# Optimization experiments

Measured on AMD Instinct MI355X. Metric: run time of the kernel, lower is better.

## Reference

```python
import jax, jax.numpy as jnp
import numpy as np
import math

SR = 16000
FFT = 1024
WIN = 640
HOP = 320
NMEL = 40
NCEP = 13
B = 1024
NS = 16000
F_MIN = 0.0
F_MAX = 8000.0
LIFT_L = 22.0
DELTA_N = 2


def _linear_to_mel_weight_matrix(num_mel, num_spec_bins, sr, fmin, fmax):
    # Exact replica of tf.signal.linear_to_mel_weight_matrix (HTK mel scale).
    def hz_to_mel(f):
        return 1127.0 * np.log1p(np.asarray(f, np.float64) / 700.0)
    nyquist = sr / 2.0
    lin_freqs = np.linspace(0.0, nyquist, num_spec_bins)
    spec_mel = hz_to_mel(lin_freqs[1:])[:, None]          # drop DC bin
    edges = np.linspace(hz_to_mel(fmin), hz_to_mel(fmax), num_mel + 2)
    lower, center, upper = edges[:-2], edges[1:-1], edges[2:]
    lower_slope = (spec_mel - lower) / (center - lower)
    upper_slope = (upper - spec_mel) / (upper - center)
    w = np.maximum(0.0, np.minimum(lower_slope, upper_slope))
    w = np.pad(w, ((1, 0), (0, 0)))                       # re-add zero DC row
    return w.astype(np.float32)


def setup_inputs() -> dict:
    key = jax.random.key(0)
    waveforms = jax.random.normal(key, (B, NS), dtype=jnp.float32)
    mel_fb = jnp.asarray(_linear_to_mel_weight_matrix(NMEL, FFT // 2 + 1, SR, F_MIN, F_MAX))
    return {"waveforms": waveforms, "mel_fb": mel_fb}


def _delta(feat, N):
    # feat: (B, T, C). Replicate-pad N frames at both ends, then weighted
    # sliding-window sum with weights k in [-N..N] (vectorized, no map_fn).
    T = feat.shape[1]
    denom = 2.0 * sum(float(k * k) for k in range(1, N + 1))
    padded = jnp.concatenate(
        [jnp.repeat(feat[:, :1, :], N, axis=1), feat,
         jnp.repeat(feat[:, -1:, :], N, axis=1)], axis=1)
    acc = jnp.zeros_like(feat)
    for k in range(-N, N + 1):
        if k != 0:
            acc = acc + float(k) * padded[:, N + k:N + k + T, :]
    return acc / denom


def reference(waveforms, mel_fb):
    # --- STFT (tf.signal.stft: periodic Hann, no pad_end, zero-pad to FFT) ---
    n = jnp.arange(WIN, dtype=jnp.float32)
    window = 0.5 - 0.5 * jnp.cos(2.0 * math.pi * n / WIN)
    num_frames = 1 + (NS - WIN) // HOP                    # 49
    idx = jnp.arange(num_frames)[:, None] * HOP + jnp.arange(WIN)[None, :]
    frames = waveforms[:, idx] * window
    frames = jnp.pad(frames, ((0, 0), (0, 0), (0, FFT - WIN)))
    spec = jnp.abs(jnp.fft.rfft(frames, n=FFT, axis=-1))  # (B, T, 513)

    # --- mel + log ---
    log_mel = jnp.log(spec @ mel_fb + 1e-6)               # (B, T, NMEL)

    # --- MFCC: DCT-II scaled by rsqrt(2*NMEL), keep first NCEP coeffs ---
    m = jnp.arange(NMEL, dtype=jnp.float32)[:, None]
    k = jnp.arange(NCEP, dtype=jnp.float32)[None, :]
    dct_mat = 2.0 * jnp.cos(math.pi * (2.0 * m + 1.0) * k / (2.0 * NMEL))
    mfccs = (log_mel @ dct_mat) * (1.0 / math.sqrt(2.0 * NMEL))

    # --- liftering ---
    c = jnp.arange(NCEP, dtype=jnp.float32)
    lift = 1.0 + (LIFT_L / 2.0) * jnp.sin(math.pi * c / LIFT_L)
    mfccs = mfccs * lift

    # --- deltas and delta-deltas ---
    d1 = _delta(mfccs, DELTA_N)
    d2 = _delta(d1, DELTA_N)
    out = jnp.concatenate([mfccs, d1, d2], axis=2)        # (B, T, 3*NCEP)
    return out[..., None]                                 # (B, T, 39, 1)
```

## Files before the change

kernel.cpp:

```cpp
#include <hip/hip_runtime.h>
#include <math.h>

#define NMEL   40
#define NCEP   13
#define BATCH  1024
#define NSAMP  16000
#define NFRAME 49
#define PI_F   3.14159265358979323846f

#define WS_WIN  0
#define WS_R    640
#define WS_DT   1664
#define WS_BT   2184
#define WS_TOT  15240
#define SENT0   0x4D464343u
#define SENT1   0x9A7C55E1u

typedef _Float16 half8 __attribute__((ext_vector_type(8)));
typedef __fp16   fp16x2 __attribute__((ext_vector_type(2)));
typedef float f32x4 __attribute__((ext_vector_type(4)));
typedef float f32x2 __attribute__((ext_vector_type(2)));

#define FFT_SB() __builtin_amdgcn_sched_barrier(0x77)

__device__ __forceinline__ f32x2 cmulw(f32x2 d, float wr, float wi) {
    f32x2 sw; sw.x = -d.y; sw.y = d.x;
    return d * wr + sw * wi;
}
#define BFLYC(i0, i1, wr, wi) {            \
    f32x2 dif = zc[i0] - zc[i1];           \
    zc[i0] = zc[i0] + zc[i1];              \
    zc[i1] = cmulw(dif, (wr), (wi)); }

__device__ __forceinline__ unsigned pk_f16(float a, float b) {
    fp16x2 h = __builtin_amdgcn_cvt_pkrtz(a, b);
    union { fp16x2 h; unsigned u; } cvt; cvt.h = h;
    return cvt.u;
}

__global__ __launch_bounds__(256) void mfcc_prep(
    const float* __restrict__ mel_fb, float* __restrict__ ws, int use_sent)
{
    if (use_sent) {
        const unsigned* sw = (const unsigned*)ws;
        if (sw[WS_TOT] == SENT0 && sw[WS_TOT + 1] == SENT1) return;
    }

    const int idx = blockIdx.x * 256 + threadIdx.x;

    _Float16* bt = (_Float16*)(ws + WS_BT);
    for (int i = idx; i < 48 * 544; i += 64 * 256) {
        int n = i / 544, k = i - n * 544;
        float v = (n < NMEL && k < 513) ? mel_fb[k * NMEL + n] : 0.0f;
        bt[i] = (_Float16)v;
    }

    if (idx < 640 + 512 + 520) {
        int i = idx;
        if (i < 640) {
            ws[WS_WIN + i] = 0.5f - 0.5f * cosf(2.0f * PI_F * (float)i / 640.0f);
        } else if (i < 1152) {
            int k = i - 640;
            float s, c;
            sincosf(-2.0f * PI_F * (float)k / 1024.0f, &s, &c);
            ((float2*)(ws + WS_R))[k] = make_float2(c, s);
        } else {
            int j = i - 1152;
            int m = j / 13, c0 = j - m * 13;
            float d    = 2.0f * cosf(PI_F * (2.0f * m + 1.0f) * (float)c0 / 80.0f);
            float lift = 1.0f + 11.0f * sinf(PI_F * (float)c0 / 22.0f);
            ws[WS_DT + j] = d * 0.11180339887498949f * lift;
        }
    }

    if (use_sent && idx == 0) {
        unsigned* sw = (unsigned*)ws;
        sw[WS_TOT]     = SENT0;
        sw[WS_TOT + 1] = SENT1;
    }
}

__device__ __forceinline__ void ldFrame(float2 (&x)[5], const float* __restrict__ wave,
                                        int frame, int L)
{
    const int b = frame / NFRAME;
    const int f = frame - b * NFRAME;
    const float2* xp = (const float2*)(wave + (size_t)b * NSAMP + (size_t)f * 320);
    #pragma unroll
    for (int j = 0; j < 5; ++j) x[j] = xp[L + 64 * j];
}

__device__ __forceinline__ void phaseI(f32x2 (&zc)[8],
    const float2 (&xv)[5], const float2 (&winv)[5],
    const float2 (&twA)[4], const float2 (&twB)[2], const float2 twC)
{
    #pragma unroll
    for (int j = 0; j < 8; ++j) { zc[j].x = 0.0f; zc[j].y = 0.0f; }
    #pragma unroll
    for (int j = 0; j < 5; ++j) {
        f32x2 x; x.x = xv[j].x;   x.y = xv[j].y;
        f32x2 w; w.x = winv[j].x; w.y = winv[j].y;
        zc[j] = x * w;
    }
    #pragma unroll
    for (int j = 0; j < 4; ++j) BFLYC(j, j + 4, twA[j].x, twA[j].y);
    #pragma unroll
    for (int g = 0; g < 8; g += 4) {
        #pragma unroll
        for (int j = 0; j < 2; ++j) BFLYC(g + j, g + j + 2, twB[j].x, twB[j].y);
    }
    #pragma unroll
    for (int i0 = 0; i0 < 8; i0 += 2) BFLYC(i0, i0 + 1, twC.x, twC.y);
}

__device__ __forceinline__ void phaseII(f32x2 (&zc)[8],
    const float4 (&q)[4],
    const float2 (&twD)[4], const float2 (&twE)[2], const float2 twF)
{
    zc[0].x = q[0].x; zc[0].y = q[0].y; zc[1].x = q[0].z; zc[1].y = q[0].w;
    zc[2].x = q[1].x; zc[2].y = q[1].y; zc[3].x = q[1].z; zc[3].y = q[1].w;
    zc[4].x = q[2].x; zc[4].y = q[2].y; zc[5].x = q[2].z; zc[5].y = q[2].w;
    zc[6].x = q[3].x; zc[6].y = q[3].y; zc[7].x = q[3].z; zc[7].y = q[3].w;
    #pragma unroll
    for (int j = 0; j < 4; ++j) BFLYC(j, j + 4, twD[j].x, twD[j].y);
    #pragma unroll
    for (int g = 0; g < 8; g += 4) {
        #pragma unroll
        for (int j = 0; j < 2; ++j) BFLYC(g + j, g + j + 2, twE[j].x, twE[j].y);
    }
    #pragma unroll
    for (int i0 = 0; i0 < 8; i0 += 2) BFLYC(i0, i0 + 1, twF.x, twF.y);
}

__device__ __forceinline__ void phaseIII(f32x2 (&zc)[8], const float4 (&q)[4])
{
    zc[0].x = q[0].x; zc[0].y = q[0].y; zc[1].x = q[0].z; zc[1].y = q[0].w;
    zc[2].x = q[1].x; zc[2].y = q[1].y; zc[3].x = q[1].z; zc[3].y = q[1].w;
    zc[4].x = q[2].x; zc[4].y = q[2].y; zc[5].x = q[2].z; zc[5].y = q[2].w;
    zc[6].x = q[3].x; zc[6].y = q[3].y; zc[7].x = q[3].z; zc[7].y = q[3].w;
    const float C = 0.70710678118654752f;
    const float w8r[4] = { 1.0f,  C, 0.0f, -C };
    const float w8i[4] = { 0.0f, -C, -1.0f, -C };
    #pragma unroll
    for (int j = 0; j < 4; ++j) BFLYC(j, j + 4, w8r[j], w8i[j]);
    #pragma unroll
    for (int g = 0; g < 8; g += 4) {
        BFLYC(g + 0, g + 2, 1.0f, 0.0f);
        BFLYC(g + 1, g + 3, 0.0f, -1.0f);
    }
    #pragma unroll
    for (int i0 = 0; i0 < 8; i0 += 2) BFLYC(i0, i0 + 1, 1.0f, 0.0f);
}

__device__ __forceinline__ void wrEx1(float2* Z, const f32x2 (&zc)[8], int s, int a)
{
    #pragma unroll
    for (int j = 0; j < 8; ++j) Z[80 * j + 10 * s + a] = make_float2(zc[j].x, zc[j].y);
}

__device__ __forceinline__ void wrEx2(float2* Z, const f32x2 (&zc)[8], int s, int a)
{
    #pragma unroll
    for (int j = 0; j < 8; ++j) Z[80 * a + 10 * j + s] = make_float2(zc[j].x, zc[j].y);
}

__device__ __forceinline__ void wrEx3(float2* Z, const f32x2 (&zc)[8], int u)
{
    const int rev3t[8] = { 0, 4, 2, 6, 1, 5, 3, 7 };
    #pragma unroll
    for (int j = 0; j < 8; ++j) Z[80 * rev3t[j] + u] = make_float2(zc[j].x, zc[j].y);
}

__device__ __forceinline__ void rdEx(const float2* Z, int L, float4 (&q)[4])
{
    q[0] = *(const float4*)&Z[10 * L + 0];
    q[1] = *(const float4*)&Z[10 * L + 2];
    q[2] = *(const float4*)&Z[10 * L + 4];
    q[3] = *(const float4*)&Z[10 * L + 6];
}

__device__ __forceinline__ void rdMag(const float2* Z, int L,
    float4 (&aq)[4], float4 (&tq)[4], float2& b0)
{
    aq[0] = *(const float4*)&Z[10 * L + 0];
    aq[1] = *(const float4*)&Z[10 * L + 2];
    aq[2] = *(const float4*)&Z[10 * L + 4];
    aq[3] = *(const float4*)&Z[10 * L + 6];
    tq[0] = *(const float4*)&Z[630 - 10 * L + 0];
    tq[1] = *(const float4*)&Z[630 - 10 * L + 2];
    tq[2] = *(const float4*)&Z[630 - 10 * L + 4];
    tq[3] = *(const float4*)&Z[630 - 10 * L + 6];
    b0    = Z[640 - 10 * L];
}

__device__ __forceinline__ void magPhase(const float4 (&aq)[4], const float4 (&tq)[4],
    const float2 b0, const float2 (&twS)[8], const int L, uint4& mgpo, float& m512o)
{
    float Ax[8], Ay[8], Bx[8], By[8];
    Ax[0] = aq[0].x; Ay[0] = aq[0].y; Ax[1] = aq[0].z; Ay[1] = aq[0].w;
    Ax[2] = aq[1].x; Ay[2] = aq[1].y; Ax[3] = aq[1].z; Ay[3] = aq[1].w;
    Ax[4] = aq[2].x; Ay[4] = aq[2].y; Ax[5] = aq[2].z; Ay[5] = aq[2].w;
    Ax[6] = aq[3].x; Ay[6] = aq[3].y; Ax[7] = aq[3].z; Ay[7] = aq[3].w;
    Bx[0] = b0.x;    By[0] = b0.y;
    Bx[7] = tq[0].z; By[7] = tq[0].w;
    Bx[6] = tq[1].x; By[6] = tq[1].y;
    Bx[5] = tq[1].z; By[5] = tq[1].w;
    Bx[4] = tq[2].x; By[4] = tq[2].y;
    Bx[3] = tq[2].z; By[3] = tq[2].w;
    Bx[2] = tq[3].x; By[2] = tq[3].y;
    Bx[1] = tq[3].z; By[1] = tq[3].w;
    float mg[8];
    #pragma unroll
    for (int j = 0; j < 8; ++j) {
        float xer = 0.5f * (Ax[j] + Bx[j]), xei = 0.5f * (Ay[j] - By[j]);
        float xo  = 0.5f * (Ay[j] + By[j]), xoi = -0.5f * (Ax[j] - Bx[j]);
        float xr = xer + twS[j].x * xo - twS[j].y * xoi;
        float xi = xei + twS[j].x * xoi + twS[j].y * xo;
        mg[j] = __builtin_amdgcn_sqrtf(xr * xr + xi * xi);
    }
    if (L == 0) {
        mg[0]  = fabsf(Ax[0] + Ay[0]);
        m512o  = fabsf(Ax[0] - Ay[0]);
    }
    mgpo.x = pk_f16(mg[0], mg[1]);
    mgpo.y = pk_f16(mg[2], mg[3]);
    mgpo.z = pk_f16(mg[4], mg[5]);
    mgpo.w = pk_f16(mg[6], mg[7]);
}

__global__ __launch_bounds__(256) void mfcc_stage1(
    const float* __restrict__ wave, const float* __restrict__ ws,
    float* __restrict__ out)
{
    __shared__ __align__(16) char smem[4 * 640 * 8 + 16];
    char* smemc = smem;
    _Float16* lm = (_Float16*)(smem + 16 * 1104);

    const int tid = threadIdx.x;
    const int wv  = tid >> 6;
    const int L   = tid & 63;
    const int s   = L & 7;
    const int a   = L >> 3;

    float2* Z = (float2*)smem + wv * 640;
    const float2* R   = (const float2*)(ws + WS_R);
    const float2* win = (const float2*)(ws + WS_WIN);

    float2 twA[4], twB[2], twC, twD[4], twE[2], twF, twS[8], winv[5];
    #pragma unroll
    for (int j = 0; j < 4; ++j) twA[j] = R[2 * (L + 64 * j)];
    #pragma unroll
    for (int j = 0; j < 2; ++j) twB[j] = R[4 * (L + 64 * j)];
    twC = R[8 * L];
    #pragma unroll
    for (int j = 0; j < 4; ++j) twD[j] = R[128 * j + 16 * s];
    #pragma unroll
    for (int j = 0; j < 2; ++j) twE[j] = R[256 * j + 32 * s];
    twF = R[64 * s];
    #pragma unroll
    for (int j = 0; j < 8; ++j) twS[j] = R[8 * L + j];
    #pragma unroll
    for (int j = 0; j < 5; ++j) winv[j] = win[L + 64 * j];

    const int r6 = (int)(__brev((unsigned)L) >> 26);
    const int u  = r6 + 2 * (r6 >> 3);

    uint4 mgp0, mgp1, mgp2, mgp3;
    float m5120 = 0.0f, m5121 = 0.0f, m5122 = 0.0f, m5123 = 0.0f;

    const int fbase = blockIdx.x * 16 + wv * 4;

    float2 xA[5], xB[5];
    ldFrame(xA, wave, fbase + 0, L);
    ldFrame(xB, wave, fbase + 1, L);

    #pragma unroll 1
    for (int p = 0; p < 2; ++p) {
        float2 xA2[5], xB2[5];
        if (p == 0) {
            ldFrame(xA2, wave, fbase + 2, L);
            ldFrame(xB2, wave, fbase + 3, L);
        }

        f32x2 zcA[8], zcB[8];
        float4 qA[4], qB[4];

        phaseI(zcA, xA, winv, twA, twB, twC);
        FFT_SB();
        wrEx1(Z, zcA, s, a);
        FFT_SB();
        rdEx(Z, L, qA);
        FFT_SB();
        phaseI(zcB, xB, winv, twA, twB, twC);
        wrEx1(Z, zcB, s, a);
        FFT_SB();
        rdEx(Z, L, qB);
        FFT_SB();

        phaseII(zcA, qA, twD, twE, twF);
        wrEx2(Z, zcA, s, a);
        FFT_SB();
        rdEx(Z, L, qA);
        FFT_SB();
        phaseII(zcB, qB, twD, twE, twF);
        wrEx2(Z, zcB, s, a);
        FFT_SB();
        rdEx(Z, L, qB);
        FFT_SB();

        phaseIII(zcA, qA);
        wrEx3(Z, zcA, u);
        FFT_SB();
        float4 aqA[4], tqA[4]; float2 b0A;
        rdMag(Z, L, aqA, tqA, b0A);
        FFT_SB();
        phaseIII(zcB, qB);
        wrEx3(Z, zcB, u);
        FFT_SB();
        float4 aqB[4], tqB[4]; float2 b0B;
        rdMag(Z, L, aqB, tqB, b0B);
        FFT_SB();

        uint4 mgA, mgB;
        float mA = 0.0f, mB = 0.0f;
        magPhase(aqA, tqA, b0A, twS, L, mgA, mA);
        magPhase(aqB, tqB, b0B, twS, L, mgB, mB);
        FFT_SB();

        mgp0 = mgp2;  mgp1 = mgp3;  mgp2 = mgA;  mgp3 = mgB;
        m5120 = m5122; m5121 = m5123; m5122 = mA; m5123 = mB;

        if (p == 0) {
            #pragma unroll
            for (int j = 0; j < 5; ++j) { xA[j] = xA2[j]; xB[j] = xB2[j]; }
        }
    }

    __syncthreads();
    {
        const int row = wv * 4;
        *(uint4*)(smemc + (row + 0) * 1104 + 16 * L) = mgp0;
        *(uint4*)(smemc + (row + 1) * 1104 + 16 * L) = mgp1;
        *(uint4*)(smemc + (row + 2) * 1104 + 16 * L) = mgp2;
        *(uint4*)(smemc + (row + 3) * 1104 + 16 * L) = mgp3;
        if (L < 20) {
            unsigned v0 = (L == 0) ? pk_f16(m5120, 0.0f) : 0u;
            unsigned v1 = (L == 0) ? pk_f16(m5121, 0.0f) : 0u;
            unsigned v2 = (L == 0) ? pk_f16(m5122, 0.0f) : 0u;
            unsigned v3 = (L == 0) ? pk_f16(m5123, 0.0f) : 0u;
            *(unsigned*)(smemc + (row + 0) * 1104 + 1024 + 4 * L) = v0;
            *(unsigned*)(smemc + (row + 1) * 1104 + 1024 + 4 * L) = v1;
            *(unsigned*)(smemc + (row + 2) * 1104 + 1024 + 4 * L) = v2;
            *(unsigned*)(smemc + (row + 3) * 1104 + 1024 + 4 * L) = v3;
        }
    }
    __syncthreads();

    if (wv < 3) {
        const int nl = L & 15, q = L >> 4;
        const char* ap = smemc + nl * 1104 + q * 16;
        const _Float16* btp = (const _Float16*)(ws + WS_BT)
                              + (size_t)(wv * 16 + nl) * 544 + q * 8;
        f32x4 acc = {0.0f, 0.0f, 0.0f, 0.0f};
        #pragma unroll
        for (int kk = 0; kk < 17; ++kk) {
            half8 av = *(const half8*)(ap + kk * 64);
            half8 bv = *(const half8*)(btp + kk * 32);
            acc = __builtin_amdgcn_mfma_f32_16x16x32_f16(av, bv, acc, 0, 0, 0);
        }
        const int mel = wv * 16 + nl;
        if (mel < NMEL) {
            #pragma unroll
            for (int r = 0; r < 4; ++r) {
                int fl = q * 4 + r;
                lm[fl * NMEL + mel] = (_Float16)__logf(acc[r] + 1e-6f);
            }
        }
    }
    __syncthreads();

    if (tid < 16 * NCEP) {
        const int fl = tid / NCEP, c = tid - fl * NCEP;
        float acc = 0.0f;
        #pragma unroll
        for (int m = 0; m < NMEL; ++m)
            acc += (float)lm[fl * NMEL + m] * ws[WS_DT + m * 13 + c];
        out[(size_t)(blockIdx.x * 16 + fl) * (3 * NCEP) + c] = acc;
    }
}

__global__ __launch_bounds__(256) void mfcc_stage2(float* __restrict__ out)
{
    #define TC (NFRAME * NCEP)
    __shared__ float xs [4][TC];
    __shared__ float d1s[4][TC];

    const int wv = threadIdx.x >> 6;
    const int L  = threadIdx.x & 63;
    const int b  = blockIdx.x * 4 + wv;

    float* xw  = xs[wv];
    float* d1w = d1s[wv];
    const size_t obase = (size_t)b * NFRAME * (3 * NCEP);

    for (int i = L; i < TC; i += 64) {
        const int t = i / NCEP, c = i - t * NCEP;
        xw[i] = out[obase + t * (3 * NCEP) + c];
    }
    FFT_SB();

    for (int i = L; i < TC; i += 64) {
        const int t = i / NCEP, c = i - t * NCEP;
        float acc = 0.0f;
        #pragma unroll
        for (int k = -2; k <= 2; ++k) {
            if (k == 0) continue;
            int tt = t + k;
            tt = tt < 0 ? 0 : (tt > NFRAME - 1 ? NFRAME - 1 : tt);
            acc += (float)k * xw[tt * NCEP + c];
        }
        float d1 = acc * 0.1f;
        d1w[i] = d1;
        out[obase + t * (3 * NCEP) + NCEP + c] = d1;
    }
    FFT_SB();

    for (int i = L; i < TC; i += 64) {
        const int t = i / NCEP, c = i - t * NCEP;
        float acc = 0.0f;
        #pragma unroll
        for (int k = -2; k <= 2; ++k) {
            if (k == 0) continue;
            int tt = t + k;
            tt = tt < 0 ? 0 : (tt > NFRAME - 1 ? NFRAME - 1 : tt);
            acc += (float)k * d1w[tt * NCEP + c];
        }
        out[obase + t * (3 * NCEP) + 2 * NCEP + c] = acc * 0.1f;
    }
    #undef TC
}

extern "C" void kernel_launch(void* const* d_in, const int* in_sizes, int n_in,
                              void* d_out, int out_size, void* d_ws, size_t ws_size,
                              hipStream_t stream)
{
    const float* wave   = (const float*)d_in[0];
    const float* mel_fb = (const float*)d_in[1];
    float* out = (float*)d_out;
    float* ws  = (float*)d_ws;

    const int use_sent = (ws_size >= (size_t)(WS_TOT + 2) * 4) ? 1 : 0;

    mfcc_prep<<<64, 256, 0, stream>>>(mel_fb, ws, use_sent);
    mfcc_stage1<<<(BATCH * NFRAME) / 16, 256, 0, stream>>>(wave, ws, out);
    mfcc_stage2<<<BATCH / 4, 256, 0, stream>>>(out);
}
```

Baseline: 157.0 us.

## Compute FFT twiddles and window on the fly and process one frame at a time

Stops loading twiddle factors and the Hann window from the workspace into registers and computes them inline with hardware sin/cos intrinsics. The loop now handles one frame per iteration instead of two interleaved frames, and each frame's magnitudes go straight to a separate shared-memory region rather than being held in registers until the end. Launch bounds ask for 4 blocks per CU. The aim is to cut register pressure and raise occupancy, at the cost of more transcendental instructions, more shared memory, less instruction-level parallelism and slightly lower twiddle accuracy.

```diff
diff --git a/kernel.cpp b/kernel.cpp
--- a/kernel.cpp
+++ b/kernel.cpp
@@ -16,6 +16,14 @@
 #define SENT0   0x4D464343u
 #define SENT1   0x9A7C55E1u
 
+#define INV16    0.0625f
+#define INV32    0.03125f
+#define INV64    0.015625f
+#define INV128   0.0078125f
+#define INV256   0.00390625f
+#define INV512   0.001953125f
+#define INV1024  0.0009765625f
+
 typedef _Float16 half8 __attribute__((ext_vector_type(8)));
 typedef __fp16   fp16x2 __attribute__((ext_vector_type(2)));
 typedef float f32x4 __attribute__((ext_vector_type(4)));
@@ -36,6 +44,10 @@
     fp16x2 h = __builtin_amdgcn_cvt_pkrtz(a, b);
     union { fp16x2 h; unsigned u; } cvt; cvt.h = h;
     return cvt.u;
+}
+
+__device__ __forceinline__ float2 twid(float rev) {
+    return make_float2(__builtin_amdgcn_cosf(rev), __builtin_amdgcn_sinf(rev));
 }
 
 __global__ __launch_bounds__(256) void mfcc_prep(
@@ -90,46 +102,62 @@
     for (int j = 0; j < 5; ++j) x[j] = xp[L + 64 * j];
 }
 
-__device__ __forceinline__ void phaseI(f32x2 (&zc)[8],
-    const float2 (&xv)[5], const float2 (&winv)[5],
-    const float2 (&twA)[4], const float2 (&twB)[2], const float2 twC)
-{
+__device__ __forceinline__ void phaseIc(f32x2 (&zc)[8], const float2 (&xv)[5], int L)
+{
+    const float nb = (float)L;
     #pragma unroll
     for (int j = 0; j < 8; ++j) { zc[j].x = 0.0f; zc[j].y = 0.0f; }
     #pragma unroll
     for (int j = 0; j < 5; ++j) {
-        f32x2 x; x.x = xv[j].x;   x.y = xv[j].y;
-        f32x2 w; w.x = winv[j].x; w.y = winv[j].y;
-        zc[j] = x * w;
-    }
-    #pragma unroll
-    for (int j = 0; j < 4; ++j) BFLYC(j, j + 4, twA[j].x, twA[j].y);
-    #pragma unroll
-    for (int g = 0; g < 8; g += 4) {
-        #pragma unroll
-        for (int j = 0; j < 2; ++j) BFLYC(g + j, g + j + 2, twB[j].x, twB[j].y);
-    }
-    #pragma unroll
-    for (int i0 = 0; i0 < 8; i0 += 2) BFLYC(i0, i0 + 1, twC.x, twC.y);
-}
-
-__device__ __forceinline__ void phaseII(f32x2 (&zc)[8],
-    const float4 (&q)[4],
-    const float2 (&twD)[4], const float2 (&twE)[2], const float2 twF)
+        float n2 = (float)(L + 64 * j) * (1.0f / 320.0f);
+        float wx = 0.5f - 0.5f * __builtin_amdgcn_cosf(n2);
+        float wy = 0.5f - 0.5f * __builtin_amdgcn_cosf(n2 + (1.0f / 640.0f));
+        zc[j].x = xv[j].x * wx;
+        zc[j].y = xv[j].y * wy;
+    }
+    const float a0 = -nb * INV512;
+    #pragma unroll
+    for (int j = 0; j < 4; ++j) {
+        float2 w = twid(a0 - 0.125f * (float)j);
+        BFLYC(j, j + 4, w.x, w.y);
+    }
+    const float b0r = -nb * INV256;
+    {
+        float2 w0 = twid(b0r), w1 = twid(b0r - 0.25f);
+        BFLYC(0, 2, w0.x, w0.y); BFLYC(1, 3, w1.x, w1.y);
+        BFLYC(4, 6, w0.x, w0.y); BFLYC(5, 7, w1.x, w1.y);
+    }
+    {
+        float2 wc = twid(-nb * INV128);
+        #pragma unroll
+        for (int i0 = 0; i0 < 8; i0 += 2) BFLYC(i0, i0 + 1, wc.x, wc.y);
+    }
+}
+
+__device__ __forceinline__ void phaseIIc(f32x2 (&zc)[8], const float4 (&q)[4], int s)
 {
     zc[0].x = q[0].x; zc[0].y = q[0].y; zc[1].x = q[0].z; zc[1].y = q[0].w;
     zc[2].x = q[1].x; zc[2].y = q[1].y; zc[3].x = q[1].z; zc[3].y = q[1].w;
     zc[4].x = q[2].x; zc[4].y = q[2].y; zc[5].x = q[2].z; zc[5].y = q[2].w;
     zc[6].x = q[3].x; zc[6].y = q[3].y; zc[7].x = q[3].z; zc[7].y = q[3].w;
-    #pragma unroll
-    for (int j = 0; j < 4; ++j) BFLYC(j, j + 4, twD[j].x, twD[j].y);
-    #pragma unroll
-    for (int g = 0; g < 8; g += 4) {
-        #pragma unroll
-        for (int j = 0; j < 2; ++j) BFLYC(g + j, g + j + 2, twE[j].x, twE[j].y);
-    }
-    #pragma unroll
-    for (int i0 = 0; i0 < 8; i0 += 2) BFLYC(i0, i0 + 1, twF.x, twF.y);
+    const float fs = (float)s;
+    const float d0 = -fs * INV64;
+    #pragma unroll
+    for (int j = 0; j < 4; ++j) {
+        float2 w = twid(d0 - 0.125f * (float)j);
+        BFLYC(j, j + 4, w.x, w.y);
+    }
+    const float e0 = -fs * INV32;
+    {
+        float2 w0 = twid(e0), w1 = twid(e0 - 0.25f);
+        BFLYC(0, 2, w0.x, w0.y); BFLYC(1, 3, w1.x, w1.y);
+        BFLYC(4, 6, w0.x, w0.y); BFLYC(5, 7, w1.x, w1.y);
+    }
+    {
+        float2 wf = twid(-fs * INV16);
+        #pragma unroll
+        for (int i0 = 0; i0 < 8; i0 += 2) BFLYC(i0, i0 + 1, wf.x, wf.y);
+    }
 }
 
 __device__ __forceinline__ void phaseIII(f32x2 (&zc)[8], const float4 (&q)[4])
@@ -194,7 +222,7 @@
 }
 
 __device__ __forceinline__ void magPhase(const float4 (&aq)[4], const float4 (&tq)[4],
-    const float2 b0, const float2 (&twS)[8], const int L, uint4& mgpo, float& m512o)
+    const float2 b0, const int L, uint4& mgpo, float& m512o)
 {
     float Ax[8], Ay[8], Bx[8], By[8];
     Ax[0] = aq[0].x; Ay[0] = aq[0].y; Ax[1] = aq[0].z; Ay[1] = aq[0].w;
@@ -209,13 +237,15 @@
     Bx[3] = tq[2].z; By[3] = tq[2].w;
     Bx[2] = tq[3].x; By[2] = tq[3].y;
     Bx[1] = tq[3].z; By[1] = tq[3].w;
+    const float s0 = -(float)L * INV128;
     float mg[8];
     #pragma unroll
     for (int j = 0; j < 8; ++j) {
+        float2 tws = twid(s0 - (float)j * INV1024);
         float xer = 0.5f * (Ax[j] + Bx[j]), xei = 0.5f * (Ay[j] - By[j]);
         float xo  = 0.5f * (Ay[j] + By[j]), xoi = -0.5f * (Ax[j] - Bx[j]);
-        float xr = xer + twS[j].x * xo - twS[j].y * xoi;
-        float xi = xei + twS[j].x * xoi + twS[j].y * xo;
+        float xr = xer + tws.x * xo - tws.y * xoi;
+        float xi = xei + tws.x * xoi + tws.y * xo;
         mg[j] = __builtin_amdgcn_sqrtf(xr * xr + xi * xi);
     }
     if (L == 0) {
@@ -228,13 +258,13 @@
     mgpo.w = pk_f16(mg[6], mg[7]);
 }
 
-__global__ __launch_bounds__(256) void mfcc_stage1(
+__global__ __launch_bounds__(256, 4) void mfcc_stage1(
     const float* __restrict__ wave, const float* __restrict__ ws,
     float* __restrict__ out)
 {
-    __shared__ __align__(16) char smem[4 * 640 * 8 + 16];
-    char* smemc = smem;
-    _Float16* lm = (_Float16*)(smem + 16 * 1104);
+    __shared__ __align__(16) char smem[20480 + 16 + 16 * 1104 + 16 * 40 * 2];
+    char* magc = smem + 20496;
+    _Float16* lm = (_Float16*)(smem + 20496 + 17664);
 
     const int tid = threadIdx.x;
     const int wv  = tid >> 6;
@@ -243,124 +273,55 @@
     const int a   = L >> 3;
 
     float2* Z = (float2*)smem + wv * 640;
-    const float2* R   = (const float2*)(ws + WS_R);
-    const float2* win = (const float2*)(ws + WS_WIN);
-
-    float2 twA[4], twB[2], twC, twD[4], twE[2], twF, twS[8], winv[5];
-    #pragma unroll
-    for (int j = 0; j < 4; ++j) twA[j] = R[2 * (L + 64 * j)];
-    #pragma unroll
-    for (int j = 0; j < 2; ++j) twB[j] = R[4 * (L + 64 * j)];
-    twC = R[8 * L];
-    #pragma unroll
-    for (int j = 0; j < 4; ++j) twD[j] = R[128 * j + 16 * s];
-    #pragma unroll
-    for (int j = 0; j < 2; ++j) twE[j] = R[256 * j + 32 * s];
-    twF = R[64 * s];
-    #pragma unroll
-    for (int j = 0; j < 8; ++j) twS[j] = R[8 * L + j];
-    #pragma unroll
-    for (int j = 0; j < 5; ++j) winv[j] = win[L + 64 * j];
 
     const int r6 = (int)(__brev((unsigned)L) >> 26);
     const int u  = r6 + 2 * (r6 >> 3);
 
-    uint4 mgp0, mgp1, mgp2, mgp3;
-    float m5120 = 0.0f, m5121 = 0.0f, m5122 = 0.0f, m5123 = 0.0f;
-
     const int fbase = blockIdx.x * 16 + wv * 4;
 
-    float2 xA[5], xB[5];
-    ldFrame(xA, wave, fbase + 0, L);
-    ldFrame(xB, wave, fbase + 1, L);
+    float2 xv[5];
+    ldFrame(xv, wave, fbase, L);
 
     #pragma unroll 1
-    for (int p = 0; p < 2; ++p) {
-        float2 xA2[5], xB2[5];
-        if (p == 0) {
-            ldFrame(xA2, wave, fbase + 2, L);
-            ldFrame(xB2, wave, fbase + 3, L);
-        }
-
-        f32x2 zcA[8], zcB[8];
-        float4 qA[4], qB[4];
-
-        phaseI(zcA, xA, winv, twA, twB, twC);
-        FFT_SB();
-        wrEx1(Z, zcA, s, a);
-        FFT_SB();
-        rdEx(Z, L, qA);
-        FFT_SB();
-        phaseI(zcB, xB, winv, twA, twB, twC);
-        wrEx1(Z, zcB, s, a);
-        FFT_SB();
-        rdEx(Z, L, qB);
-        FFT_SB();
-
-        phaseII(zcA, qA, twD, twE, twF);
-        wrEx2(Z, zcA, s, a);
-        FFT_SB();
-        rdEx(Z, L, qA);
-        FFT_SB();
-        phaseII(zcB, qB, twD, twE, twF);
-        wrEx2(Z, zcB, s, a);
-        FFT_SB();
-        rdEx(Z, L, qB);
-        FFT_SB();
-
-        phaseIII(zcA, qA);
-        wrEx3(Z, zcA, u);
-        FFT_SB();
-        float4 aqA[4], tqA[4]; float2 b0A;
-        rdMag(Z, L, aqA, tqA, b0A);
-        FFT_SB();
-        phaseIII(zcB, qB);
-        wrEx3(Z, zcB, u);
-        FFT_SB();
-        float4 aqB[4], tqB[4]; float2 b0B;
-        rdMag(Z, L, aqB, tqB, b0B);
-        FFT_SB();
-
-        uint4 mgA, mgB;
-        float mA = 0.0f, mB = 0.0f;
-        magPhase(aqA, tqA, b0A, twS, L, mgA, mA);
-        magPhase(aqB, tqB, b0B, twS, L, mgB, mB);
-        FFT_SB();
-
-        mgp0 = mgp2;  mgp1 = mgp3;  mgp2 = mgA;  mgp3 = mgB;
-        m5120 = m5122; m5121 = m5123; m5122 = mA; m5123 = mB;
-
-        if (p == 0) {
-            #pragma unroll
-            for (int j = 0; j < 5; ++j) { xA[j] = xA2[j]; xB[j] = xB2[j]; }
-        }
+    for (int fi = 0; fi < 4; ++fi) {
+        f32x2 zc[8];
+        phaseIc(zc, xv, L);
+        FFT_SB();
+        wrEx1(Z, zc, s, a);
+        FFT_SB();
+        if (fi < 3) ldFrame(xv, wave, fbase + fi + 1, L);
+        float4 q[4];
+        rdEx(Z, L, q);
+        FFT_SB();
+        phaseIIc(zc, q, s);
+        wrEx2(Z, zc, s, a);
+        FFT_SB();
+        rdEx(Z, L, q);
+        FFT_SB();
+        phaseIII(zc, q);
+        wrEx3(Z, zc, u);
+        FFT_SB();
+        float4 aq[4], tq[4]; float2 b0;
+        rdMag(Z, L, aq, tq, b0);
+        FFT_SB();
+        uint4 mg; float m512 = 0.0f;
+        magPhase(aq, tq, b0, L, mg, m512);
+        char* mrow = magc + (wv * 4 + fi) * 1104;
+        *(uint4*)(mrow + 16 * L) = mg;
+        if (L < 20) {
+            unsigned v = (L == 0) ? pk_f16(m512, 0.0f) : 0u;
+            *(unsigned*)(mrow + 1024 + 4 * L) = v;
+        }
+        FFT_SB();
     }
 
     __syncthreads();
-    {
-        const int row = wv * 4;
-        *(uint4*)(smemc + (row + 0) * 1104 + 16 * L) = mgp0;
-        *(uint4*)(smemc + (row + 1) * 1104 + 16 * L) = mgp1;
-        *(uint4*)(smemc + (row + 2) * 1104 + 16 * L) = mgp2;
-        *(uint4*)(smemc + (row + 3) * 1104 + 16 * L) = mgp3;
-        if (L < 20) {
-            unsigned v0 = (L == 0) ? pk_f16(m5120, 0.0f) : 0u;
-            unsigned v1 = (L == 0) ? pk_f16(m5121, 0.0f) : 0u;
-            unsigned v2 = (L == 0) ? pk_f16(m5122, 0.0f) : 0u;
-            unsigned v3 = (L == 0) ? pk_f16(m5123, 0.0f) : 0u;
-            *(unsigned*)(smemc + (row + 0) * 1104 + 1024 + 4 * L) = v0;
-            *(unsigned*)(smemc + (row + 1) * 1104 + 1024 + 4 * L) = v1;
-            *(unsigned*)(smemc + (row + 2) * 1104 + 1024 + 4 * L) = v2;
-            *(unsigned*)(smemc + (row + 3) * 1104 + 1024 + 4 * L) = v3;
-        }
-    }
-    __syncthreads();
 
     if (wv < 3) {
-        const int nl = L & 15, q = L >> 4;
-        const char* ap = smemc + nl * 1104 + q * 16;
+        const int nl = L & 15, qq = L >> 4;
+        const char* ap = magc + nl * 1104 + qq * 16;
         const _Float16* btp = (const _Float16*)(ws + WS_BT)
-                              + (size_t)(wv * 16 + nl) * 544 + q * 8;
+                              + (size_t)(wv * 16 + nl) * 544 + qq * 8;
         f32x4 acc = {0.0f, 0.0f, 0.0f, 0.0f};
         #pragma unroll
         for (int kk = 0; kk < 17; ++kk) {
@@ -372,7 +333,7 @@
         if (mel < NMEL) {
             #pragma unroll
             for (int r = 0; r < 4; ++r) {
-                int fl = q * 4 + r;
+                int fl = qq * 4 + r;
                 lm[fl * NMEL + mel] = (_Float16)__logf(acc[r] + 1e-6f);
             }
         }
```

Measured after the change: 158.3 us. No clear change (+0.8%).
